# Kernel optimization log

Hardware: AMD Instinct MI355X
Metric: run time of the kernel (lower is better)

## Reference

```python
import jax, jax.numpy as jnp
import numpy as np

N_NODES = 10000
N_EDGES = 160000
IN_FEAT = 1024
H_FEAT = 1024
NUM_CLASSES = 64


def setup_inputs() -> dict:
    key = jax.random.key(0)
    ks = jax.random.split(key, 8)
    h = jax.random.normal(ks[0], (N_NODES, IN_FEAT), dtype=jnp.float32)
    src = jax.random.randint(ks[1], (N_EDGES,), 0, N_NODES, dtype=jnp.int32)
    dst = jax.random.randint(ks[2], (N_EDGES,), 0, N_NODES, dtype=jnp.int32)
    # Xavier-ish scaled weights (DGL uses xavier_uniform for GraphConv)
    W1 = jax.random.normal(ks[3], (IN_FEAT, H_FEAT), dtype=jnp.float32) * (1.0 / np.sqrt(IN_FEAT))
    b1 = jnp.zeros((H_FEAT,), dtype=jnp.float32)
    W2 = jax.random.normal(ks[4], (H_FEAT, H_FEAT), dtype=jnp.float32) * (1.0 / np.sqrt(H_FEAT))
    b2 = jnp.zeros((H_FEAT,), dtype=jnp.float32)
    W3 = jax.random.normal(ks[5], (H_FEAT, NUM_CLASSES), dtype=jnp.float32) * (1.0 / np.sqrt(H_FEAT))
    b3 = jnp.zeros((NUM_CLASSES,), dtype=jnp.float32)
    return {"h": h, "src": src, "dst": dst,
            "W1": W1, "b1": b1, "W2": W2, "b2": b2, "W3": W3, "b3": b3}


def _graph_conv(src, dst, norm_src, norm_dst, x, W, b):
    """DGL GraphConv with norm='both':
    out = D_dst^{-1/2} * sum_{(u,v) in E} (D_src^{-1/2} * x)_u  @ W + b
    """
    xs = x * norm_src[:, None]                     # [N, d] scaled source feats
    msg = xs[src]                                  # [E, d] gather
    agg = jax.ops.segment_sum(msg, dst, num_segments=N_NODES)  # [N, d] scatter-add
    agg = agg * norm_dst[:, None]
    return agg @ W + b


def reference(h, src, dst, W1, b1, W2, b2, W3, b3):
    ones = jnp.ones((N_EDGES,), dtype=jnp.float32)
    deg_out = jax.ops.segment_sum(ones, src, num_segments=N_NODES)  # out-degree of src
    deg_in = jax.ops.segment_sum(ones, dst, num_segments=N_NODES)   # in-degree of dst
    norm_src = jnp.clip(deg_out, 1.0, None) ** -0.5
    norm_dst = jnp.clip(deg_in, 1.0, None) ** -0.5

    x = _graph_conv(src, dst, norm_src, norm_dst, h, W1, b1)
    x = jax.nn.relu(x)
    x = _graph_conv(src, dst, norm_src, norm_dst, x, W2, b2)
    x = jax.nn.relu(x)
    x = _graph_conv(src, dst, norm_src, norm_dst, x, W3, b3)
    return x
```

## Files before the change

kernel.cpp:

```cpp
#include <hip/hip_runtime.h>

constexpr int NN   = 10000;
constexpr int NE   = 160000;
constexpr int F    = 1024;
constexpr int C3   = 64;
constexpr int MPAD = 10112;

typedef __attribute__((ext_vector_type(8))) short short8;
typedef __attribute__((ext_vector_type(8))) unsigned short ushort8v;
typedef __attribute__((ext_vector_type(4))) float floatx4;

__device__ __forceinline__ unsigned short f2bf(float f) {
    union { float f; unsigned u; } v; v.f = f;
    unsigned r = v.u + 0x7fff + ((v.u >> 16) & 1);
    return (unsigned short)(r >> 16);
}
__device__ __forceinline__ float bf2f(unsigned short u) {
    union { unsigned u; float f; } v; v.u = ((unsigned)u) << 16;
    return v.f;
}

__device__ __forceinline__ void gl_lds16(const void* g, void* l) {
    __builtin_amdgcn_global_load_lds(
        (const __attribute__((address_space(1))) unsigned int*)g,
        (__attribute__((address_space(3))) unsigned int*)l, 16, 0, 0);
}


__global__ __launch_bounds__(256) void k_degree(const int* __restrict__ src,
                                                const int* __restrict__ dst,
                                                int* __restrict__ deg_out,
                                                int* __restrict__ deg_in) {
    int e = blockIdx.x * 256 + threadIdx.x;
    if (e < NE) {
        atomicAdd(&deg_out[src[e]], 1);
        atomicAdd(&deg_in[dst[e]], 1);
    }
}

__global__ __launch_bounds__(1024) void k_scan(const int* __restrict__ deg_in,
                                               const int* __restrict__ deg_out,
                                               int* __restrict__ row_ptr,
                                               int* __restrict__ cursor,
                                               float* __restrict__ norm_src,
                                               float* __restrict__ norm_dst) {
    constexpr int CH = 10;
    __shared__ int sums[1024];
    const int tid = threadIdx.x;
    int local[CH];
    int tsum = 0;
#pragma unroll
    for (int j = 0; j < CH; ++j) {
        int idx = tid * CH + j;
        int v = (idx < NN) ? deg_in[idx] : 0;
        local[j] = v;
        tsum += v;
        if (idx < MPAD) {
            norm_src[idx] = rsqrtf(fmaxf((float)deg_out[idx], 1.0f));
            norm_dst[idx] = rsqrtf(fmaxf((float)deg_in[idx], 1.0f));
        }
    }
    sums[tid] = tsum;
    __syncthreads();
    for (int off = 1; off < 1024; off <<= 1) {
        int v = (tid >= off) ? sums[tid - off] : 0;
        __syncthreads();
        sums[tid] += v;
        __syncthreads();
    }
    int run = sums[tid] - tsum;
#pragma unroll
    for (int j = 0; j < CH; ++j) {
        int idx = tid * CH + j;
        if (idx < NN) {
            row_ptr[idx] = run;
            cursor[idx]  = run;
        }
        run += local[j];
    }
    if (tid == 1023) row_ptr[NN] = sums[1023];
}

__global__ __launch_bounds__(256) void k_bucket(const int* __restrict__ src,
                                                const int* __restrict__ dst,
                                                int* __restrict__ cursor,
                                                int* __restrict__ csr_src) {
    int e = blockIdx.x * 256 + threadIdx.x;
    if (e < NE) {
        int slot = atomicAdd(&cursor[dst[e]], 1);
        csr_src[slot] = src[e];
    }
}

__global__ __launch_bounds__(256) void k_wconv_all(const float* __restrict__ W1,
                                                   const float* __restrict__ W2,
                                                   const float* __restrict__ W3,
                                                   unsigned short* __restrict__ Wt1,
                                                   unsigned short* __restrict__ Wt2,
                                                   unsigned short* __restrict__ Wt3) {
    __shared__ float tile[32][33];
    const float* W; unsigned short* Wt; int N, n0, k0;
    int b = blockIdx.x;
    if (b < 1024)      { W = W1; Wt = Wt1; N = F;  n0 = (b & 31) * 32;          k0 = (b >> 5) * 32; }
    else if (b < 2048) { b -= 1024; W = W2; Wt = Wt2; N = F;  n0 = (b & 31) * 32; k0 = (b >> 5) * 32; }
    else               { b -= 2048; W = W3; Wt = Wt3; N = C3; n0 = (b & 1) * 32;  k0 = (b >> 1) * 32; }
    const int tx = threadIdx.x & 31, ty = threadIdx.x >> 5;
#pragma unroll
    for (int i = 0; i < 32; i += 8)
        tile[ty + i][tx] = W[(size_t)(k0 + ty + i) * N + n0 + tx];
    __syncthreads();
#pragma unroll
    for (int i = 0; i < 32; i += 8)
        Wt[(size_t)(n0 + ty + i) * F + k0 + tx] = f2bf(tile[tx][ty + i]);
}


__global__ __launch_bounds__(256) void k_hcvt(const float* __restrict__ h,
                                              const float* __restrict__ norm_src,
                                              unsigned short* __restrict__ hb) {
    int idx = blockIdx.x * 256 + threadIdx.x;
    int v = idx >> 7, f8 = (idx & 127) * 8;
    float ns = norm_src[v];
    const float4 a = *(const float4*)(h + (size_t)v * F + f8);
    const float4 b = *(const float4*)(h + (size_t)v * F + f8 + 4);
    ushort8v o;
    o[0] = f2bf(ns * a.x); o[1] = f2bf(ns * a.y);
    o[2] = f2bf(ns * a.z); o[3] = f2bf(ns * a.w);
    o[4] = f2bf(ns * b.x); o[5] = f2bf(ns * b.y);
    o[6] = f2bf(ns * b.z); o[7] = f2bf(ns * b.w);
    *(ushort8v*)(hb + (size_t)v * F + f8) = o;
}

__global__ __launch_bounds__(256) void k_aggb(const unsigned short* __restrict__ xb,
                                              const int* __restrict__ row_ptr,
                                              const int* __restrict__ csr_src,
                                              unsigned short* __restrict__ aggb) {
    const int c = blockIdx.x & 7;
    const int g = blockIdx.x >> 3;
    const int v = g * 16 + (threadIdx.x >> 4);
    const int f8 = c * 128 + (threadIdx.x & 15) * 8;
    const int lo = row_ptr[v], hi = row_ptr[v + 1];
    float acc[8] = {0.f, 0.f, 0.f, 0.f, 0.f, 0.f, 0.f, 0.f};
    int i = lo;
    for (; i + 4 <= hi; i += 4) {
        int s0 = csr_src[i],     s1 = csr_src[i + 1];
        int s2 = csr_src[i + 2], s3 = csr_src[i + 3];
        ushort8v x0 = *(const ushort8v*)(xb + (size_t)s0 * F + f8);
        ushort8v x1 = *(const ushort8v*)(xb + (size_t)s1 * F + f8);
        ushort8v x2 = *(const ushort8v*)(xb + (size_t)s2 * F + f8);
        ushort8v x3 = *(const ushort8v*)(xb + (size_t)s3 * F + f8);
#pragma unroll
        for (int j = 0; j < 8; ++j) acc[j] += bf2f(x0[j]);
#pragma unroll
        for (int j = 0; j < 8; ++j) acc[j] += bf2f(x1[j]);
#pragma unroll
        for (int j = 0; j < 8; ++j) acc[j] += bf2f(x2[j]);
#pragma unroll
        for (int j = 0; j < 8; ++j) acc[j] += bf2f(x3[j]);
    }
    for (; i < hi; ++i) {
        int s = csr_src[i];
        ushort8v xv = *(const ushort8v*)(xb + (size_t)s * F + f8);
#pragma unroll
        for (int j = 0; j < 8; ++j) acc[j] += bf2f(xv[j]);
    }
    ushort8v o;
#pragma unroll
    for (int j = 0; j < 8; ++j) o[j] = f2bf(acc[j]);
    *(ushort8v*)(aggb + (size_t)v * F + f8) = o;
}

__global__ __launch_bounds__(256) void k_agg64(const float* __restrict__ z,
                                               const int* __restrict__ row_ptr,
                                               const int* __restrict__ csr_src,
                                               const float* __restrict__ norm_dst,
                                               const float* __restrict__ b3,
                                               float* __restrict__ out) {
    const int v = blockIdx.x * 16 + (threadIdx.x >> 4);
    if (v >= NN) return;
    const int f4 = (threadIdx.x & 15) * 4;
    const int lo = row_ptr[v], hi = row_ptr[v + 1];
    float4 acc = {0.f, 0.f, 0.f, 0.f};
    int i = lo;
    for (; i + 2 <= hi; i += 2) {
        int s0 = csr_src[i], s1 = csr_src[i + 1];
        float4 z0 = *(const float4*)(z + (size_t)s0 * C3 + f4);
        float4 z1 = *(const float4*)(z + (size_t)s1 * C3 + f4);
        acc.x += z0.x; acc.y += z0.y; acc.z += z0.z; acc.w += z0.w;
        acc.x += z1.x; acc.y += z1.y; acc.z += z1.z; acc.w += z1.w;
    }
    if (i < hi) {
        int s = csr_src[i];
        float4 zv = *(const float4*)(z + (size_t)s * C3 + f4);
        acc.x += zv.x; acc.y += zv.y; acc.z += zv.z; acc.w += zv.w;
    }
    float nd = norm_dst[v];
    float4 bv = *(const float4*)(b3 + f4);
    float4 o;
    o.x = acc.x * nd + bv.x; o.y = acc.y * nd + bv.y;
    o.z = acc.z * nd + bv.z; o.w = acc.w * nd + bv.w;
    *(float4*)(out + (size_t)v * C3 + f4) = o;
}

__global__ __launch_bounds__(512) void k_gemm_bf16(
        const unsigned short* __restrict__ A,
        const unsigned short* __restrict__ Bt,
        const float* __restrict__ bias,
        const float* __restrict__ rs1,
        const float* __restrict__ rs2,
        unsigned short* __restrict__ Cb) {
    __shared__ short As[2][128 * 32];
    __shared__ short Bs[2][128 * 32];
    const int t = threadIdx.x, lane = t & 63, wid = t >> 6;
    const int m0 = blockIdx.x * 128, n0 = blockIdx.y * 128;
    const int wm0 = (wid & 1) * 64, wn0 = (wid >> 1) * 32;
    const int lr = lane & 15, q = lane >> 4;

    const int rS  = wid * 16 + (lane >> 2);
    const int sS  = (((lane & 3) ^ ((rS >> 1) & 3)) * 8);
    const unsigned short* aSrc = A  + (size_t)(m0 + rS) * F + sS;
    const unsigned short* bSrc = Bt + (size_t)(n0 + rS) * F + sS;
    short* aDst = &As[0][wid * 512];
    short* bDst = &Bs[0][wid * 512];

    const short* ap[4];
    const short* bp[2];
#pragma unroll
    for (int mb = 0; mb < 4; ++mb) {
        int m = wm0 + mb * 16 + lr;
        ap[mb] = &As[0][m * 32 + (q ^ ((m >> 1) & 3)) * 8];
    }
#pragma unroll
    for (int nb = 0; nb < 2; ++nb) {
        int n = wn0 + nb * 16 + lr;
        bp[nb] = &Bs[0][n * 32 + (q ^ ((n >> 1) & 3)) * 8];
    }

    floatx4 acc[4][2] = {};

    gl_lds16(aSrc, aDst);
    gl_lds16(bSrc, bDst);

    for (int kt = 0; kt < F / 32; ++kt) {
        const int buf = kt & 1;
        __syncthreads();
        if (kt + 1 < F / 32) {
            int k0 = (kt + 1) * 32;
            gl_lds16(aSrc + k0, aDst + (buf ^ 1) * (128 * 32));
            gl_lds16(bSrc + k0, bDst + (buf ^ 1) * (128 * 32));
        }
        const int bo = buf * (128 * 32);
        short8 af[4], bf[2];
#pragma unroll
        for (int mb = 0; mb < 4; ++mb) af[mb] = *(const short8*)(ap[mb] + bo);
#pragma unroll
        for (int nb = 0; nb < 2; ++nb) bf[nb] = *(const short8*)(bp[nb] + bo);
#pragma unroll
        for (int mb = 0; mb < 4; ++mb)
#pragma unroll
            for (int nb = 0; nb < 2; ++nb)
                acc[mb][nb] = __builtin_amdgcn_mfma_f32_16x16x32_bf16(
                    af[mb], bf[nb], acc[mb][nb], 0, 0, 0);
    }

    float s1[4][4], s2[4][4];
#pragma unroll
    for (int mb = 0; mb < 4; ++mb)
#pragma unroll
        for (int r = 0; r < 4; ++r) {
            int row = m0 + wm0 + mb * 16 + q * 4 + r;
            s1[mb][r] = rs1[row];
            s2[mb][r] = rs2[row];
        }
#pragma unroll
    for (int nb = 0; nb < 2; ++nb) {
        int col = n0 + wn0 + nb * 16 + lr;
        float bv = bias[col];
#pragma unroll
        for (int mb = 0; mb < 4; ++mb)
#pragma unroll
            for (int r = 0; r < 4; ++r) {
                int row = m0 + wm0 + mb * 16 + q * 4 + r;
                float v = fmaxf(acc[mb][nb][r] * s1[mb][r] + bv, 0.f) * s2[mb][r];
                Cb[(size_t)row * F + col] = f2bf(v);
            }
    }
}

__global__ __launch_bounds__(256) void k_gemm3(
        const unsigned short* __restrict__ A,
        const unsigned short* __restrict__ Bt,
        float* __restrict__ Z) {
    __shared__ short As3[2][64 * 32];
    __shared__ short Bs3[2][64 * 32];
    const int t = threadIdx.x, lane = t & 63, wid = t >> 6;
    const int m0 = blockIdx.x * 64;
    const int lr = lane & 15, q = lane >> 4;

    const int r = wid * 16 + (lane >> 2);
    const int soff = (((lane & 3) ^ ((r >> 1) & 3)) * 8);
    const unsigned short* aSrc = A  + (size_t)(m0 + r) * F + soff;
    const unsigned short* bSrc = Bt + (size_t)r * F + soff;

    const short* ap;
    {
        int m = wid * 16 + lr;
        ap = &As3[0][m * 32 + (q ^ ((m >> 1) & 3)) * 8];
    }
    const short* bp[4];
#pragma unroll
    for (int nb = 0; nb < 4; ++nb) {
        int n = nb * 16 + lr;
        bp[nb] = &Bs3[0][n * 32 + (q ^ ((n >> 1) & 3)) * 8];
    }

    floatx4 acc[4] = {};

    gl_lds16(aSrc, &As3[0][wid * 512]);
    gl_lds16(bSrc, &Bs3[0][wid * 512]);

    for (int kt = 0; kt < F / 32; ++kt) {
        const int buf = kt & 1;
        __syncthreads();
        if (kt + 1 < F / 32) {
            int k0 = (kt + 1) * 32;
            gl_lds16(aSrc + k0, &As3[buf ^ 1][wid * 512]);
            gl_lds16(bSrc + k0, &Bs3[buf ^ 1][wid * 512]);
        }
        const int bo = buf * (64 * 32);
        short8 af = *(const short8*)(ap + bo);
        short8 bf[4];
#pragma unroll
        for (int nb = 0; nb < 4; ++nb) bf[nb] = *(const short8*)(bp[nb] + bo);
#pragma unroll
        for (int nb = 0; nb < 4; ++nb)
            acc[nb] = __builtin_amdgcn_mfma_f32_16x16x32_bf16(af, bf[nb], acc[nb], 0, 0, 0);
    }

#pragma unroll
    for (int nb = 0; nb < 4; ++nb) {
        int col = nb * 16 + lr;
#pragma unroll
        for (int ri = 0; ri < 4; ++ri) {
            int row = m0 + wid * 16 + q * 4 + ri;
            Z[(size_t)row * C3 + col] = acc[nb][ri];
        }
    }
}


extern "C" void kernel_launch(void* const* d_in, const int* in_sizes, int n_in,
                              void* d_out, int out_size, void* d_ws, size_t ws_size,
                              hipStream_t stream) {
    const float* h   = (const float*)d_in[0];
    const int*   src = (const int*)d_in[1];
    const int*   dst = (const int*)d_in[2];
    const float* W1  = (const float*)d_in[3];
    const float* b1  = (const float*)d_in[4];
    const float* W2  = (const float*)d_in[5];
    const float* b2  = (const float*)d_in[6];
    const float* W3  = (const float*)d_in[7];
    const float* b3  = (const float*)d_in[8];
    float* out = (float*)d_out;

    char* ws = (char*)d_ws;
    int*   deg_out  = (int*)ws;                       ws += MPAD * 4;
    int*   deg_in   = (int*)ws;                       ws += MPAD * 4;
    float* norm_src = (float*)ws;                     ws += MPAD * 4;
    float* norm_dst = (float*)ws;                     ws += MPAD * 4;
    int*   row_ptr  = (int*)ws;                       ws += (NN + 1) * 4;
    int*   cursor   = (int*)ws;                       ws += NN * 4;
    int*   csr_src  = (int*)ws;                       ws += NE * 4;
    ws = (char*)(((size_t)ws + 255) & ~(size_t)255);
    unsigned short* hb   = (unsigned short*)ws;       ws += (size_t)MPAD * F * 2;
    unsigned short* aggb = (unsigned short*)ws;       ws += (size_t)MPAD * F * 2;
    unsigned short* xb   = (unsigned short*)ws;       ws += (size_t)MPAD * F * 2;
    unsigned short* Wt1  = (unsigned short*)ws;       ws += (size_t)F * F * 2;
    unsigned short* Wt2  = (unsigned short*)ws;       ws += (size_t)F * F * 2;
    unsigned short* Wt3  = (unsigned short*)ws;       ws += (size_t)C3 * F * 2;
    float* z3       = (float*)ws;

    hipMemsetAsync(deg_out, 0, 2 * MPAD * sizeof(int), stream);
    k_degree<<<(NE + 255) / 256, 256, 0, stream>>>(src, dst, deg_out, deg_in);
    k_scan<<<1, 1024, 0, stream>>>(deg_in, deg_out, row_ptr, cursor, norm_src, norm_dst);
    k_bucket<<<(NE + 255) / 256, 256, 0, stream>>>(src, dst, cursor, csr_src);
    k_wconv_all<<<2112, 256, 0, stream>>>(W1, W2, W3, Wt1, Wt2, Wt3);
    k_hcvt<<<NN * 128 / 256, 256, 0, stream>>>(h, norm_src, hb);

    k_aggb<<<(NN / 16) * 8, 256, 0, stream>>>(hb, row_ptr, csr_src, aggb);
    k_gemm_bf16<<<dim3(MPAD / 128, F / 128), 512, 0, stream>>>(aggb, Wt1, b1, norm_dst, norm_src, xb);

    k_aggb<<<(NN / 16) * 8, 256, 0, stream>>>(xb, row_ptr, csr_src, aggb);
    k_gemm_bf16<<<dim3(MPAD / 128, F / 128), 512, 0, stream>>>(aggb, Wt2, b2, norm_dst, norm_src, xb);

    k_gemm3<<<MPAD / 64, 256, 0, stream>>>(xb, Wt3, z3);
    k_agg64<<<(NN + 15) / 16, 256, 0, stream>>>(z3, row_ptr, csr_src, norm_dst, b3, out);
}
```

Before: 296.9 us.

## Merge prep kernels by block range and double GEMM K-tile to 64

The degree count and weight conversion are merged into one launch, and the CSR bucketing and input conversion into another, with blocks dispatched by index range to cut launch count and let independent work overlap. The bf16 GEMM now stages 64-wide K tiles instead of 32, with a new XOR swizzle over 8 chunks. This halves the number of barriers and loop iterations per tile but doubles LDS use per block, which may lower occupancy.

```diff
diff --git a/kernel.cpp b/kernel.cpp
--- a/kernel.cpp
+++ b/kernel.cpp
@@ -27,16 +27,39 @@
 }
 
 
-__global__ __launch_bounds__(256) void k_degree(const int* __restrict__ src,
-                                                const int* __restrict__ dst,
-                                                int* __restrict__ deg_out,
-                                                int* __restrict__ deg_in) {
-    int e = blockIdx.x * 256 + threadIdx.x;
-    if (e < NE) {
+__global__ __launch_bounds__(256) void k_prep1(const int* __restrict__ src,
+                                               const int* __restrict__ dst,
+                                               int* __restrict__ deg_out,
+                                               int* __restrict__ deg_in,
+                                               const float* __restrict__ W1,
+                                               const float* __restrict__ W2,
+                                               const float* __restrict__ W3,
+                                               unsigned short* __restrict__ Wt1,
+                                               unsigned short* __restrict__ Wt2,
+                                               unsigned short* __restrict__ Wt3) {
+    __shared__ float tile[32][33];
+    int b = blockIdx.x;
+    if (b < 625) {
+        int e = b * 256 + threadIdx.x;
         atomicAdd(&deg_out[src[e]], 1);
         atomicAdd(&deg_in[dst[e]], 1);
-    }
-}
+        return;
+    }
+    b -= 625;
+    const float* W; unsigned short* Wt; int N, n0, k0;
+    if (b < 1024)      { W = W1; Wt = Wt1; N = F;  n0 = (b & 31) * 32;         k0 = (b >> 5) * 32; }
+    else if (b < 2048) { b -= 1024; W = W2; Wt = Wt2; N = F;  n0 = (b & 31) * 32; k0 = (b >> 5) * 32; }
+    else               { b -= 2048; W = W3; Wt = Wt3; N = C3; n0 = (b & 1) * 32;  k0 = (b >> 1) * 32; }
+    const int tx = threadIdx.x & 31, ty = threadIdx.x >> 5;
+#pragma unroll
+    for (int i = 0; i < 32; i += 8)
+        tile[ty + i][tx] = W[(size_t)(k0 + ty + i) * N + n0 + tx];
+    __syncthreads();
+#pragma unroll
+    for (int i = 0; i < 32; i += 8)
+        Wt[(size_t)(n0 + ty + i) * F + k0 + tx] = f2bf(tile[tx][ty + i]);
+}
+
 
 __global__ __launch_bounds__(1024) void k_scan(const int* __restrict__ deg_in,
                                                const int* __restrict__ deg_out,
@@ -81,53 +104,32 @@
     if (tid == 1023) row_ptr[NN] = sums[1023];
 }
 
-__global__ __launch_bounds__(256) void k_bucket(const int* __restrict__ src,
-                                                const int* __restrict__ dst,
-                                                int* __restrict__ cursor,
-                                                int* __restrict__ csr_src) {
-    int e = blockIdx.x * 256 + threadIdx.x;
-    if (e < NE) {
+
+__global__ __launch_bounds__(256) void k_prep2(const int* __restrict__ src,
+                                               const int* __restrict__ dst,
+                                               int* __restrict__ cursor,
+                                               int* __restrict__ csr_src,
+                                               const float* __restrict__ h,
+                                               const float* __restrict__ norm_src,
+                                               unsigned short* __restrict__ hb) {
+    int b = blockIdx.x;
+    if (b < 625) {
+        int e = b * 256 + threadIdx.x;
         int slot = atomicAdd(&cursor[dst[e]], 1);
         csr_src[slot] = src[e];
-    }
-}
-
-__global__ __launch_bounds__(256) void k_wconv_all(const float* __restrict__ W1,
-                                                   const float* __restrict__ W2,
-                                                   const float* __restrict__ W3,
-                                                   unsigned short* __restrict__ Wt1,
-                                                   unsigned short* __restrict__ Wt2,
-                                                   unsigned short* __restrict__ Wt3) {
-    __shared__ float tile[32][33];
-    const float* W; unsigned short* Wt; int N, n0, k0;
-    int b = blockIdx.x;
-    if (b < 1024)      { W = W1; Wt = Wt1; N = F;  n0 = (b & 31) * 32;          k0 = (b >> 5) * 32; }
-    else if (b < 2048) { b -= 1024; W = W2; Wt = Wt2; N = F;  n0 = (b & 31) * 32; k0 = (b >> 5) * 32; }
-    else               { b -= 2048; W = W3; Wt = Wt3; N = C3; n0 = (b & 1) * 32;  k0 = (b >> 1) * 32; }
-    const int tx = threadIdx.x & 31, ty = threadIdx.x >> 5;
-#pragma unroll
-    for (int i = 0; i < 32; i += 8)
-        tile[ty + i][tx] = W[(size_t)(k0 + ty + i) * N + n0 + tx];
-    __syncthreads();
-#pragma unroll
-    for (int i = 0; i < 32; i += 8)
-        Wt[(size_t)(n0 + ty + i) * F + k0 + tx] = f2bf(tile[tx][ty + i]);
-}
-
-
-__global__ __launch_bounds__(256) void k_hcvt(const float* __restrict__ h,
-                                              const float* __restrict__ norm_src,
-                                              unsigned short* __restrict__ hb) {
-    int idx = blockIdx.x * 256 + threadIdx.x;
+        return;
+    }
+    b -= 625;
+    int idx = b * 256 + threadIdx.x;
     int v = idx >> 7, f8 = (idx & 127) * 8;
     float ns = norm_src[v];
     const float4 a = *(const float4*)(h + (size_t)v * F + f8);
-    const float4 b = *(const float4*)(h + (size_t)v * F + f8 + 4);
+    const float4 c = *(const float4*)(h + (size_t)v * F + f8 + 4);
     ushort8v o;
     o[0] = f2bf(ns * a.x); o[1] = f2bf(ns * a.y);
     o[2] = f2bf(ns * a.z); o[3] = f2bf(ns * a.w);
-    o[4] = f2bf(ns * b.x); o[5] = f2bf(ns * b.y);
-    o[6] = f2bf(ns * b.z); o[7] = f2bf(ns * b.w);
+    o[4] = f2bf(ns * c.x); o[5] = f2bf(ns * c.y);
+    o[6] = f2bf(ns * c.z); o[7] = f2bf(ns * c.w);
     *(ushort8v*)(hb + (size_t)v * F + f8) = o;
 }
 
@@ -209,58 +211,65 @@
         const float* __restrict__ rs1,
         const float* __restrict__ rs2,
         unsigned short* __restrict__ Cb) {
-    __shared__ short As[2][128 * 32];
-    __shared__ short Bs[2][128 * 32];
+    __shared__ short As[2][128 * 64];
+    __shared__ short Bs[2][128 * 64];
     const int t = threadIdx.x, lane = t & 63, wid = t >> 6;
     const int m0 = blockIdx.x * 128, n0 = blockIdx.y * 128;
     const int wm0 = (wid & 1) * 64, wn0 = (wid >> 1) * 32;
     const int lr = lane & 15, q = lane >> 4;
 
-    const int rS  = wid * 16 + (lane >> 2);
-    const int sS  = (((lane & 3) ^ ((rS >> 1) & 3)) * 8);
-    const unsigned short* aSrc = A  + (size_t)(m0 + rS) * F + sS;
-    const unsigned short* bSrc = Bt + (size_t)(n0 + rS) * F + sS;
-    short* aDst = &As[0][wid * 512];
-    short* bDst = &Bs[0][wid * 512];
-
-    const short* ap[4];
-    const short* bp[2];
-#pragma unroll
-    for (int mb = 0; mb < 4; ++mb) {
-        int m = wm0 + mb * 16 + lr;
-        ap[mb] = &As[0][m * 32 + (q ^ ((m >> 1) & 3)) * 8];
-    }
-#pragma unroll
-    for (int nb = 0; nb < 2; ++nb) {
-        int n = wn0 + nb * 16 + lr;
-        bp[nb] = &Bs[0][n * 32 + (q ^ ((n >> 1) & 3)) * 8];
-    }
+    const int srow = wid * 16 + (lane >> 3);
+    const int schk = (lane & 7) ^ (lane >> 3);
+    const unsigned short* aS = A  + (size_t)(m0 + srow) * F + schk * 8;
+    const unsigned short* bS = Bt + (size_t)(n0 + srow) * F + schk * 8;
+    short* aD = &As[0][wid * 1024];
+    short* bD = &Bs[0][wid * 1024];
+
+    int moff[4], noff[2];
+#pragma unroll
+    for (int mb = 0; mb < 4; ++mb) moff[mb] = (wm0 + mb * 16 + lr) * 64;
+#pragma unroll
+    for (int nb = 0; nb < 2; ++nb) noff[nb] = (wn0 + nb * 16 + lr) * 64;
+    const int swz = lr & 7;
 
     floatx4 acc[4][2] = {};
 
-    gl_lds16(aSrc, aDst);
-    gl_lds16(bSrc, bDst);
-
-    for (int kt = 0; kt < F / 32; ++kt) {
+    gl_lds16(aS,         aD);
+    gl_lds16(aS + 8 * F, aD + 512);
+    gl_lds16(bS,         bD);
+    gl_lds16(bS + 8 * F, bD + 512);
+
+    for (int kt = 0; kt < F / 64; ++kt) {
         const int buf = kt & 1;
         __syncthreads();
-        if (kt + 1 < F / 32) {
-            int k0 = (kt + 1) * 32;
-            gl_lds16(aSrc + k0, aDst + (buf ^ 1) * (128 * 32));
-            gl_lds16(bSrc + k0, bDst + (buf ^ 1) * (128 * 32));
-        }
-        const int bo = buf * (128 * 32);
-        short8 af[4], bf[2];
-#pragma unroll
-        for (int mb = 0; mb < 4; ++mb) af[mb] = *(const short8*)(ap[mb] + bo);
-#pragma unroll
-        for (int nb = 0; nb < 2; ++nb) bf[nb] = *(const short8*)(bp[nb] + bo);
-#pragma unroll
-        for (int mb = 0; mb < 4; ++mb)
+        if (kt + 1 < F / 64) {
+            const int k0 = (kt + 1) * 64;
+            short* a2 = aD + (buf ^ 1) * (128 * 64);
+            short* b2 = bD + (buf ^ 1) * (128 * 64);
+            gl_lds16(aS + k0,         a2);
+            gl_lds16(aS + 8 * F + k0, a2 + 512);
+            gl_lds16(bS + k0,         b2);
+            gl_lds16(bS + 8 * F + k0, b2 + 512);
+        }
+        const short* Ab = &As[buf][0];
+        const short* Bb = &Bs[buf][0];
+#pragma unroll
+        for (int s = 0; s < 2; ++s) {
+            const int cq = (s * 4 + q) ^ swz;
+            short8 af[4], bf[2];
+#pragma unroll
+            for (int mb = 0; mb < 4; ++mb)
+                af[mb] = *(const short8*)&Ab[moff[mb] + cq * 8];
 #pragma unroll
             for (int nb = 0; nb < 2; ++nb)
-                acc[mb][nb] = __builtin_amdgcn_mfma_f32_16x16x32_bf16(
-                    af[mb], bf[nb], acc[mb][nb], 0, 0, 0);
+                bf[nb] = *(const short8*)&Bb[noff[nb] + cq * 8];
+#pragma unroll
+            for (int mb = 0; mb < 4; ++mb)
+#pragma unroll
+                for (int nb = 0; nb < 2; ++nb)
+                    acc[mb][nb] = __builtin_amdgcn_mfma_f32_16x16x32_bf16(
+                        af[mb], bf[nb], acc[mb][nb], 0, 0, 0);
+        }
     }
 
     float s1[4][4], s2[4][4];
@@ -381,11 +390,10 @@
     float* z3       = (float*)ws;
 
     hipMemsetAsync(deg_out, 0, 2 * MPAD * sizeof(int), stream);
-    k_degree<<<(NE + 255) / 256, 256, 0, stream>>>(src, dst, deg_out, deg_in);
+    k_prep1<<<625 + 2112, 256, 0, stream>>>(src, dst, deg_out, deg_in,
+                                            W1, W2, W3, Wt1, Wt2, Wt3);
     k_scan<<<1, 1024, 0, stream>>>(deg_in, deg_out, row_ptr, cursor, norm_src, norm_dst);
-    k_bucket<<<(NE + 255) / 256, 256, 0, stream>>>(src, dst, cursor, csr_src);
-    k_wconv_all<<<2112, 256, 0, stream>>>(W1, W2, W3, Wt1, Wt2, Wt3);
-    k_hcvt<<<NN * 128 / 256, 256, 0, stream>>>(h, norm_src, hb);
+    k_prep2<<<625 + 5000, 256, 0, stream>>>(src, dst, cursor, csr_src, h, norm_src, hb);
 
     k_aggb<<<(NN / 16) * 8, 256, 0, stream>>>(hb, row_ptr, csr_src, aggb);
     k_gemm_bf16<<<dim3(MPAD / 128, F / 128), 512, 0, stream>>>(aggb, Wt1, b1, norm_dst, norm_src, xb);
```

After: 334.6 us. +12.7%, slower.

## Merge preprocessing kernels and unroll gather-aggregation loop by eight

Applied to the files above, without the earlier changes.

Five preprocessing launches become two. Degree counting is merged with the weight transpose and convert, and CSR bucketing is merged with the scaled h-to-bf16 conversion, each grid split by block index. This removes launch gaps and lets independent work overlap. Separately, the gather-aggregate loop now issues eight row loads per iteration instead of four, exposing more memory-level parallelism at the cost of more registers.

```diff
diff --git a/kernel.cpp b/kernel.cpp
--- a/kernel.cpp
+++ b/kernel.cpp
@@ -27,16 +27,39 @@
 }
 
 
-__global__ __launch_bounds__(256) void k_degree(const int* __restrict__ src,
-                                                const int* __restrict__ dst,
-                                                int* __restrict__ deg_out,
-                                                int* __restrict__ deg_in) {
-    int e = blockIdx.x * 256 + threadIdx.x;
-    if (e < NE) {
+__global__ __launch_bounds__(256) void k_prep1(const int* __restrict__ src,
+                                               const int* __restrict__ dst,
+                                               int* __restrict__ deg_out,
+                                               int* __restrict__ deg_in,
+                                               const float* __restrict__ W1,
+                                               const float* __restrict__ W2,
+                                               const float* __restrict__ W3,
+                                               unsigned short* __restrict__ Wt1,
+                                               unsigned short* __restrict__ Wt2,
+                                               unsigned short* __restrict__ Wt3) {
+    __shared__ float tile[32][33];
+    int b = blockIdx.x;
+    if (b < 625) {
+        int e = b * 256 + threadIdx.x;
         atomicAdd(&deg_out[src[e]], 1);
         atomicAdd(&deg_in[dst[e]], 1);
-    }
-}
+        return;
+    }
+    b -= 625;
+    const float* W; unsigned short* Wt; int N, n0, k0;
+    if (b < 1024)      { W = W1; Wt = Wt1; N = F;  n0 = (b & 31) * 32;         k0 = (b >> 5) * 32; }
+    else if (b < 2048) { b -= 1024; W = W2; Wt = Wt2; N = F;  n0 = (b & 31) * 32; k0 = (b >> 5) * 32; }
+    else               { b -= 2048; W = W3; Wt = Wt3; N = C3; n0 = (b & 1) * 32;  k0 = (b >> 1) * 32; }
+    const int tx = threadIdx.x & 31, ty = threadIdx.x >> 5;
+#pragma unroll
+    for (int i = 0; i < 32; i += 8)
+        tile[ty + i][tx] = W[(size_t)(k0 + ty + i) * N + n0 + tx];
+    __syncthreads();
+#pragma unroll
+    for (int i = 0; i < 32; i += 8)
+        Wt[(size_t)(n0 + ty + i) * F + k0 + tx] = f2bf(tile[tx][ty + i]);
+}
+
 
 __global__ __launch_bounds__(1024) void k_scan(const int* __restrict__ deg_in,
                                                const int* __restrict__ deg_out,
@@ -81,53 +104,32 @@
     if (tid == 1023) row_ptr[NN] = sums[1023];
 }
 
-__global__ __launch_bounds__(256) void k_bucket(const int* __restrict__ src,
-                                                const int* __restrict__ dst,
-                                                int* __restrict__ cursor,
-                                                int* __restrict__ csr_src) {
-    int e = blockIdx.x * 256 + threadIdx.x;
-    if (e < NE) {
+
+__global__ __launch_bounds__(256) void k_prep2(const int* __restrict__ src,
+                                               const int* __restrict__ dst,
+                                               int* __restrict__ cursor,
+                                               int* __restrict__ csr_src,
+                                               const float* __restrict__ h,
+                                               const float* __restrict__ norm_src,
+                                               unsigned short* __restrict__ hb) {
+    int b = blockIdx.x;
+    if (b < 625) {
+        int e = b * 256 + threadIdx.x;
         int slot = atomicAdd(&cursor[dst[e]], 1);
         csr_src[slot] = src[e];
-    }
-}
-
-__global__ __launch_bounds__(256) void k_wconv_all(const float* __restrict__ W1,
-                                                   const float* __restrict__ W2,
-                                                   const float* __restrict__ W3,
-                                                   unsigned short* __restrict__ Wt1,
-                                                   unsigned short* __restrict__ Wt2,
-                                                   unsigned short* __restrict__ Wt3) {
-    __shared__ float tile[32][33];
-    const float* W; unsigned short* Wt; int N, n0, k0;
-    int b = blockIdx.x;
-    if (b < 1024)      { W = W1; Wt = Wt1; N = F;  n0 = (b & 31) * 32;          k0 = (b >> 5) * 32; }
-    else if (b < 2048) { b -= 1024; W = W2; Wt = Wt2; N = F;  n0 = (b & 31) * 32; k0 = (b >> 5) * 32; }
-    else               { b -= 2048; W = W3; Wt = Wt3; N = C3; n0 = (b & 1) * 32;  k0 = (b >> 1) * 32; }
-    const int tx = threadIdx.x & 31, ty = threadIdx.x >> 5;
-#pragma unroll
-    for (int i = 0; i < 32; i += 8)
-        tile[ty + i][tx] = W[(size_t)(k0 + ty + i) * N + n0 + tx];
-    __syncthreads();
-#pragma unroll
-    for (int i = 0; i < 32; i += 8)
-        Wt[(size_t)(n0 + ty + i) * F + k0 + tx] = f2bf(tile[tx][ty + i]);
-}
-
-
-__global__ __launch_bounds__(256) void k_hcvt(const float* __restrict__ h,
-                                              const float* __restrict__ norm_src,
-                                              unsigned short* __restrict__ hb) {
-    int idx = blockIdx.x * 256 + threadIdx.x;
+        return;
+    }
+    b -= 625;
+    int idx = b * 256 + threadIdx.x;
     int v = idx >> 7, f8 = (idx & 127) * 8;
     float ns = norm_src[v];
     const float4 a = *(const float4*)(h + (size_t)v * F + f8);
-    const float4 b = *(const float4*)(h + (size_t)v * F + f8 + 4);
+    const float4 c = *(const float4*)(h + (size_t)v * F + f8 + 4);
     ushort8v o;
     o[0] = f2bf(ns * a.x); o[1] = f2bf(ns * a.y);
     o[2] = f2bf(ns * a.z); o[3] = f2bf(ns * a.w);
-    o[4] = f2bf(ns * b.x); o[5] = f2bf(ns * b.y);
-    o[6] = f2bf(ns * b.z); o[7] = f2bf(ns * b.w);
+    o[4] = f2bf(ns * c.x); o[5] = f2bf(ns * c.y);
+    o[6] = f2bf(ns * c.z); o[7] = f2bf(ns * c.w);
     *(ushort8v*)(hb + (size_t)v * F + f8) = o;
 }
 
@@ -142,23 +144,29 @@
     const int lo = row_ptr[v], hi = row_ptr[v + 1];
     float acc[8] = {0.f, 0.f, 0.f, 0.f, 0.f, 0.f, 0.f, 0.f};
     int i = lo;
-    for (; i + 4 <= hi; i += 4) {
-        int s0 = csr_src[i],     s1 = csr_src[i + 1];
-        int s2 = csr_src[i + 2], s3 = csr_src[i + 3];
+    for (; i + 8 <= hi; i += 8) {
+        int s[8];
+#pragma unroll
+        for (int u = 0; u < 8; ++u) s[u] = csr_src[i + u];
+        ushort8v x[8];
+#pragma unroll
+        for (int u = 0; u < 8; ++u)
+            x[u] = *(const ushort8v*)(xb + (size_t)s[u] * F + f8);
+#pragma unroll
+        for (int u = 0; u < 8; ++u)
+#pragma unroll
+            for (int j = 0; j < 8; ++j) acc[j] += bf2f(x[u][j]);
+    }
+    for (; i + 2 <= hi; i += 2) {
+        int s0 = csr_src[i], s1 = csr_src[i + 1];
         ushort8v x0 = *(const ushort8v*)(xb + (size_t)s0 * F + f8);
         ushort8v x1 = *(const ushort8v*)(xb + (size_t)s1 * F + f8);
-        ushort8v x2 = *(const ushort8v*)(xb + (size_t)s2 * F + f8);
-        ushort8v x3 = *(const ushort8v*)(xb + (size_t)s3 * F + f8);
 #pragma unroll
         for (int j = 0; j < 8; ++j) acc[j] += bf2f(x0[j]);
 #pragma unroll
         for (int j = 0; j < 8; ++j) acc[j] += bf2f(x1[j]);
-#pragma unroll
-        for (int j = 0; j < 8; ++j) acc[j] += bf2f(x2[j]);
-#pragma unroll
-        for (int j = 0; j < 8; ++j) acc[j] += bf2f(x3[j]);
-    }
-    for (; i < hi; ++i) {
+    }
+    if (i < hi) {
         int s = csr_src[i];
         ushort8v xv = *(const ushort8v*)(xb + (size_t)s * F + f8);
 #pragma unroll
@@ -381,11 +389,10 @@
     float* z3       = (float*)ws;
 
     hipMemsetAsync(deg_out, 0, 2 * MPAD * sizeof(int), stream);
-    k_degree<<<(NE + 255) / 256, 256, 0, stream>>>(src, dst, deg_out, deg_in);
+    k_prep1<<<625 + 2112, 256, 0, stream>>>(src, dst, deg_out, deg_in,
+                                            W1, W2, W3, Wt1, Wt2, Wt3);
     k_scan<<<1, 1024, 0, stream>>>(deg_in, deg_out, row_ptr, cursor, norm_src, norm_dst);
-    k_bucket<<<(NE + 255) / 256, 256, 0, stream>>>(src, dst, cursor, csr_src);
-    k_wconv_all<<<2112, 256, 0, stream>>>(W1, W2, W3, Wt1, Wt2, Wt3);
-    k_hcvt<<<NN * 128 / 256, 256, 0, stream>>>(h, norm_src, hb);
+    k_prep2<<<625 + 5000, 256, 0, stream>>>(src, dst, cursor, csr_src, h, norm_src, hb);
 
     k_aggb<<<(NN / 16) * 8, 256, 0, stream>>>(hb, row_ptr, csr_src, aggb);
     k_gemm_bf16<<<dim3(MPAD / 128, F / 128), 512, 0, stream>>>(aggb, Wt1, b1, norm_dst, norm_src, xb);
```

After: 298.2 us (median of 2 runs). No clear change (+0.4%).
